# Kernel tuning notes

Measured on AMD Instinct MI355X. Metric: run time of the kernel, lower is better.

Reference implementation:

```python
import jax, jax.numpy as jnp
import numpy as np

N_NODES, N_EDGES, FEA_DIM, H_DIM, N_LAYER, N_GRAPHS, LABEL_DIM = 50000, 600000, 128, 256, 3, 256, 2


def setup_inputs() -> dict:
    key = jax.random.key(0)
    ks = jax.random.split(key, 8)
    x = jax.random.normal(ks[0], (N_NODES, FEA_DIM), jnp.float32)
    edge_index = jax.random.randint(ks[1], (2, N_EDGES), 0, N_NODES, dtype=jnp.int64)
    batch = jnp.sort(jax.random.randint(ks[2], (N_NODES,), 0, N_GRAPHS, dtype=jnp.int64))
    Wg = jax.random.normal(ks[3], (N_LAYER, FEA_DIM, FEA_DIM), jnp.float32) / np.sqrt(FEA_DIM)
    bg = jnp.zeros((N_LAYER, FEA_DIM), jnp.float32)
    w1 = jax.random.normal(ks[4], (FEA_DIM, H_DIM), jnp.float32) / np.sqrt(FEA_DIM)
    b1 = jnp.zeros((H_DIM,), jnp.float32)
    w2 = jax.random.normal(ks[5], (H_DIM, LABEL_DIM), jnp.float32) / np.sqrt(H_DIM)
    b2 = jnp.zeros((LABEL_DIM,), jnp.float32)
    return dict(x=x, Wg=Wg, bg=bg, w1=w1, b1=b1, w2=w2, b2=b2,
                edge_index=edge_index, batch=batch)


def reference(x, Wg, bg, w1, b1, w2, b2, edge_index, batch):
    N = x.shape[0]
    # --- GCN normalization with self-loops (PyG GCNConv default) ---
    loop = jnp.arange(N, dtype=edge_index.dtype)
    src = jnp.concatenate([edge_index[0], loop])  # [E+N]
    dst = jnp.concatenate([edge_index[1], loop])
    deg = jax.ops.segment_sum(jnp.ones_like(src, x.dtype), dst, num_segments=N)
    dinv = jnp.where(deg > 0, jax.lax.rsqrt(jnp.maximum(deg, 1.0)), 0.0)
    norm = dinv[src] * dinv[dst]  # [E+N]
    # --- stacked GCNConv + ReLU ---
    for l in range(Wg.shape[0]):
        h = x @ Wg[l]                              # [N, D] linear transform
        msg = h[src] * norm[:, None]               # gather + edge scale
        x = jax.ops.segment_sum(msg, dst, num_segments=N) + bg[l]  # scatter-add
        x = jax.nn.relu(x)
    # --- global mean pool over graphs ---
    sums = jax.ops.segment_sum(x, batch, num_segments=N_GRAPHS)
    counts = jax.ops.segment_sum(jnp.ones((N, 1), x.dtype), batch, num_segments=N_GRAPHS)
    pooled = sums / jnp.maximum(counts, 1.0)       # [G, D]
    # --- MLP head ---
    h = jax.nn.relu(pooled @ w1 + b1)
    return h @ w2 + b2                             # [G, label_dim]
```

## Files before the change

kernel.cpp:

```cpp
#include <hip/hip_runtime.h>
#include <hip/hip_bf16.h>

#define N_NODES 50000
#define N_EDGES 600000
#define FEA_DIM 128
#define H_DIM 256
#define N_LAYER 3
#define N_GRAPHS 256
#define LABEL_DIM 2

#define SCAN_NB ((N_NODES + 255) / 256)
#define GEMM_NB ((N_NODES + 63) / 64)
#define EDGE_NB ((N_EDGES + 255) / 256)
#define AGG_NB (((N_NODES + 7) / 8) * 2)


__global__ __launch_bounds__(256) void k_count(const int* __restrict__ dst, int* __restrict__ counts) {
    int e = blockIdx.x * 256 + threadIdx.x;
    if (e < N_EDGES) atomicAdd(&counts[dst[e]], 1);
}


__device__ __forceinline__ void gemm_body(const float* __restrict__ X, const float* __restrict__ W,
                                          float* __restrict__ H, int M, int tile) {
    __shared__ float a_s[32][68];
    __shared__ float b_s[32][128];
    const int tid = threadIdx.x;
    const int row_g = tid >> 4;
    const int col_g = tid & 15;
    const int row_base = tile * 64;
    float acc[4][8] = {};

    for (int kt = 0; kt < 4; ++kt) {
        const int k0 = kt * 32;
#pragma unroll
        for (int j = 0; j < 2; ++j) {
            int id = tid + j * 256;
            int m = id >> 3;
            int kq = (id & 7) << 2;
            float4 v = make_float4(0.f, 0.f, 0.f, 0.f);
            int gr = row_base + m;
            if (gr < M) v = *(const float4*)(X + gr * 128 + k0 + kq);
            a_s[kq + 0][m] = v.x; a_s[kq + 1][m] = v.y;
            a_s[kq + 2][m] = v.z; a_s[kq + 3][m] = v.w;
        }
#pragma unroll
        for (int j = 0; j < 4; ++j) {
            int id = tid + j * 256;
            int k = id >> 5;
            int n = (id & 31) << 2;
            *(float4*)(&b_s[k][n]) = *(const float4*)(W + (k0 + k) * 128 + n);
        }
        __syncthreads();
#pragma unroll 8
        for (int k = 0; k < 32; ++k) {
            float4 a0 = *(const float4*)(&a_s[k][row_g * 4]);
            float4 b0 = *(const float4*)(&b_s[k][col_g * 4]);
            float4 b1 = *(const float4*)(&b_s[k][64 + col_g * 4]);
            float av[4] = {a0.x, a0.y, a0.z, a0.w};
            float bv[8] = {b0.x, b0.y, b0.z, b0.w, b1.x, b1.y, b1.z, b1.w};
#pragma unroll
            for (int i = 0; i < 4; ++i)
#pragma unroll
                for (int jj = 0; jj < 8; ++jj) acc[i][jj] += av[i] * bv[jj];
        }
        __syncthreads();
    }
#pragma unroll
    for (int i = 0; i < 4; ++i) {
        int gr = row_base + row_g * 4 + i;
        if (gr < M) {
            float4 o0 = {acc[i][0], acc[i][1], acc[i][2], acc[i][3]};
            float4 o1 = {acc[i][4], acc[i][5], acc[i][6], acc[i][7]};
            *(float4*)(H + gr * 128 + col_g * 4) = o0;
            *(float4*)(H + gr * 128 + 64 + col_g * 4) = o1;
        }
    }
}

__global__ __launch_bounds__(256) void k_gemm(const float* __restrict__ X, const float* __restrict__ W,
                                              float* __restrict__ H, int M) {
    gemm_body(X, W, H, M, blockIdx.x);
}

__global__ __launch_bounds__(256) void k_gemm0_fill(const float* __restrict__ X, const float* __restrict__ W,
                                                    float* __restrict__ H,
                                                    const int* __restrict__ src, const int* __restrict__ dst,
                                                    const int* __restrict__ row_ptr, int* __restrict__ cursor,
                                                    int* __restrict__ col) {
    if (blockIdx.x < GEMM_NB) {
        gemm_body(X, W, H, N_NODES, blockIdx.x);
    } else {
        int e = (blockIdx.x - GEMM_NB) * 256 + threadIdx.x;
        if (e < N_EDGES) {
            int s = src[e], d = dst[e];
            int p = row_ptr[d] + atomicAdd(&cursor[d], 1);
            col[p] = s;
        }
    }
}


__global__ __launch_bounds__(256) void k_partial(const int* __restrict__ counts, int* __restrict__ partial) {
    int g = blockIdx.x * 256 + threadIdx.x;
    int v = (g < N_NODES) ? counts[g] : 0;
#pragma unroll
    for (int off = 32; off > 0; off >>= 1) v += __shfl_down(v, off);
    __shared__ int ws[4];
    int lane = threadIdx.x & 63, wid = threadIdx.x >> 6;
    if (lane == 0) ws[wid] = v;
    __syncthreads();
    if (threadIdx.x == 0) partial[blockIdx.x] = ws[0] + ws[1] + ws[2] + ws[3];
}

__global__ __launch_bounds__(256) void k_rowptr(const int* __restrict__ counts, const int* __restrict__ partial,
                                                int* __restrict__ row_ptr, float* __restrict__ dinv,
                                                int* __restrict__ cursor) {
    __shared__ int sp[256];
    __shared__ int s[256];
    int tid = threadIdx.x;
    sp[tid] = (tid < SCAN_NB) ? partial[tid] : 0;
    __syncthreads();
#pragma unroll
    for (int off = 1; off < 256; off <<= 1) {
        int t = (tid >= off) ? sp[tid - off] : 0;
        __syncthreads();
        sp[tid] += t;
        __syncthreads();
    }
    int block_off = (blockIdx.x == 0) ? 0 : sp[blockIdx.x - 1];

    int g = blockIdx.x * 256 + tid;
    int c = (g < N_NODES) ? counts[g] : 0;
    s[tid] = c;
    __syncthreads();
#pragma unroll
    for (int off = 1; off < 256; off <<= 1) {
        int t = (tid >= off) ? s[tid - off] : 0;
        __syncthreads();
        s[tid] += t;
        __syncthreads();
    }
    if (g < N_NODES) {
        row_ptr[g] = block_off + s[tid] - c;
        dinv[g] = rsqrtf((float)c + 1.0f);
        cursor[g] = 0;
    }
    if (blockIdx.x == 0 && tid == 0) row_ptr[N_NODES] = sp[SCAN_NB - 1];
}


__global__ __launch_bounds__(256) void k_agg(const float* __restrict__ H, const float* __restrict__ bgl,
                                             const int* __restrict__ row_ptr, const int* __restrict__ col,
                                             const float* __restrict__ dinv,
                                             float* __restrict__ Xo) {
    const int b = blockIdx.x;
    const int half = b & 1;
    const int unit = threadIdx.x >> 5;
    const int fl = threadIdx.x & 31;
    const int i = (b >> 1) * 8 + unit;
    if (i >= N_NODES) return;
    const int fo = half * 32 + fl;
    const float2* H2 = (const float2*)H;
    const float di = dinv[i];
    float2 h = H2[(size_t)i * 64 + fo];
    float2 acc;
    acc.x = h.x * di * di;
    acc.y = h.y * di * di;
    const int p0 = row_ptr[i], p1 = row_ptr[i + 1];
    for (int base = p0; base < p1; base += 32) {
        int m = p1 - base; if (m > 32) m = 32;
        int sc = 0; float wc = 0.f;
        if (fl < m) { sc = col[base + fl]; wc = dinv[sc] * di; }
        for (int j = 0; j < m; j += 8) {
            int cnt = m - j; if (cnt > 8) cnt = 8;
            float2 hbuf[8]; float wbuf[8];
#pragma unroll
            for (int t = 0; t < 8; ++t) {
                if (t < cnt) {
                    int s = __shfl(sc, j + t, 32);
                    wbuf[t] = __shfl(wc, j + t, 32);
                    hbuf[t] = H2[(size_t)s * 64 + fo];
                }
            }
#pragma unroll
            for (int t = 0; t < 8; ++t) {
                if (t < cnt) {
                    acc.x += hbuf[t].x * wbuf[t];
                    acc.y += hbuf[t].y * wbuf[t];
                }
            }
        }
    }
    float2 bb = ((const float2*)bgl)[fo];
    float2 o;
    o.x = fmaxf(acc.x + bb.x, 0.f);
    o.y = fmaxf(acc.y + bb.y, 0.f);
    ((float2*)Xo)[(size_t)i * 64 + fo] = o;
}


__global__ __launch_bounds__(256) void k_poolmlp(const float* __restrict__ X, const int* __restrict__ batch,
                                                 const float* __restrict__ w1, const float* __restrict__ b1,
                                                 const float* __restrict__ w2, const float* __restrict__ b2,
                                                 float* __restrict__ out) {
    __shared__ int s_lo, s_hi;
    __shared__ float red[256];
    __shared__ float xs[128];
    __shared__ float hs[256];
    int g = blockIdx.x, tid = threadIdx.x;
    if (tid == 0) {
        int lo = 0, hi = N_NODES;
        while (lo < hi) { int mid = (lo + hi) >> 1; if (batch[mid] < g) lo = mid + 1; else hi = mid; }
        s_lo = lo;
        int lo2 = lo, hi2 = N_NODES;
        while (lo2 < hi2) { int mid = (lo2 + hi2) >> 1; if (batch[mid] < g + 1) lo2 = mid + 1; else hi2 = mid; }
        s_hi = lo2;
    }
    __syncthreads();
    int lo = s_lo, hi = s_hi;
    int f = tid & 127, half = tid >> 7;
    float acc = 0.f;
    for (int r = lo + half; r < hi; r += 2) acc += X[r * 128 + f];
    red[tid] = acc;
    __syncthreads();
    if (tid < 128) {
        int cnt = hi - lo;
        xs[tid] = (red[tid] + red[tid + 128]) / (float)(cnt > 0 ? cnt : 1);
    }
    __syncthreads();
    float a1 = b1[tid];
#pragma unroll 8
    for (int k = 0; k < 128; ++k) a1 += xs[k] * w1[k * H_DIM + tid];
    hs[tid] = fmaxf(a1, 0.f);
    __syncthreads();
    int j = tid >> 7, t2 = tid & 127;
    float p = hs[t2] * w2[t2 * LABEL_DIM + j] + hs[t2 + 128] * w2[(t2 + 128) * LABEL_DIM + j];
    red[tid] = p;
    __syncthreads();
    for (int s2 = 64; s2 > 0; s2 >>= 1) {
        if (t2 < s2) red[tid] += red[tid + s2];
        __syncthreads();
    }
    if (t2 == 0) out[g * LABEL_DIM + j] = red[tid] + b2[j];
}


extern "C" void kernel_launch(void* const* d_in, const int* in_sizes, int n_in,
                              void* d_out, int out_size, void* d_ws, size_t ws_size,
                              hipStream_t stream) {
    const float* x   = (const float*)d_in[0];
    const float* Wg  = (const float*)d_in[1];
    const float* bg  = (const float*)d_in[2];
    const float* w1  = (const float*)d_in[3];
    const float* b1  = (const float*)d_in[4];
    const float* w2  = (const float*)d_in[5];
    const float* b2  = (const float*)d_in[6];
    const int* eidx  = (const int*)d_in[7];
    const int* batch = (const int*)d_in[8];
    float* out = (float*)d_out;

    const int* src = eidx;
    const int* dst = eidx + N_EDGES;

    char* ws = (char*)d_ws;
    size_t off = 0;
    float* A = (float*)(ws + off); off += (size_t)N_NODES * FEA_DIM * 4;
    float* B = (float*)(ws + off); off += (size_t)N_NODES * FEA_DIM * 4;
    int*   col = (int*)(ws + off); off += (size_t)N_EDGES * 4;
    int*   row_ptr = (int*)(ws + off); off += 200704;
    int*   cursor  = (int*)(ws + off); off += 200704;
    int*   counts  = (int*)(ws + off); off += 200704;
    float* dinv    = (float*)(ws + off); off += 200704;
    int*   partial = (int*)(ws + off); off += 4096;

    hipMemsetAsync(counts, 0, 200704, stream);
    k_count<<<EDGE_NB, 256, 0, stream>>>(dst, counts);
    k_partial<<<SCAN_NB, 256, 0, stream>>>(counts, partial);
    k_rowptr<<<SCAN_NB, 256, 0, stream>>>(counts, partial, row_ptr, dinv, cursor);
    k_gemm0_fill<<<GEMM_NB + EDGE_NB, 256, 0, stream>>>(x, Wg, B, src, dst, row_ptr, cursor, col);

    k_agg<<<AGG_NB, 256, 0, stream>>>(B, bg + 0 * FEA_DIM, row_ptr, col, dinv, A);
    for (int l = 1; l < N_LAYER; ++l) {
        k_gemm<<<GEMM_NB, 256, 0, stream>>>(A, Wg + (size_t)l * FEA_DIM * FEA_DIM, B, N_NODES);
        k_agg<<<AGG_NB, 256, 0, stream>>>(B, bg + (size_t)l * FEA_DIM, row_ptr, col, dinv, A);
    }
    k_poolmlp<<<N_GRAPHS, 256, 0, stream>>>(A, batch, w1, b1, w2, b2, out);
}
```

Measured before the change: 374.9 us.

## Store GEMM output in feature-chunked planes and split aggregation across eight chunks

The GEMM now writes H as eight planes of 16 floats per node, each plane covering all nodes, instead of row-major 128-wide rows. The aggregation kernel assigns each block one 16-float feature chunk for 32 nodes, so each node is handled by an 8-lane group. Each gathered neighbour row is a contiguous 64-byte segment within a plane. This aims to keep a plane's working set (about 3.2 MB) resident in cache during the random gathers. In exchange, each gather fetches less data per transaction, the edge-list and dinv reads are repeated eight times per node, and the loop walks neighbours in chunks of 8.

```diff
diff --git a/kernel.cpp b/kernel.cpp
--- a/kernel.cpp
+++ b/kernel.cpp
@@ -12,7 +12,7 @@
 #define SCAN_NB ((N_NODES + 255) / 256)
 #define GEMM_NB ((N_NODES + 63) / 64)
 #define EDGE_NB ((N_EDGES + 255) / 256)
-#define AGG_NB (((N_NODES + 7) / 8) * 2)
+#define AGG_NB (((N_NODES + 31) / 32) * 8)
 
 
 __global__ __launch_bounds__(256) void k_count(const int* __restrict__ dst, int* __restrict__ counts) {
@@ -66,14 +66,16 @@
         }
         __syncthreads();
     }
+    const int p0 = col_g >> 2;
+    const int o0 = (col_g & 3) * 4;
 #pragma unroll
     for (int i = 0; i < 4; ++i) {
         int gr = row_base + row_g * 4 + i;
         if (gr < M) {
-            float4 o0 = {acc[i][0], acc[i][1], acc[i][2], acc[i][3]};
-            float4 o1 = {acc[i][4], acc[i][5], acc[i][6], acc[i][7]};
-            *(float4*)(H + gr * 128 + col_g * 4) = o0;
-            *(float4*)(H + gr * 128 + 64 + col_g * 4) = o1;
+            float4 v0 = {acc[i][0], acc[i][1], acc[i][2], acc[i][3]};
+            float4 v1 = {acc[i][4], acc[i][5], acc[i][6], acc[i][7]};
+            *(float4*)(H + ((size_t)p0 * N_NODES + gr) * 16 + o0) = v0;
+            *(float4*)(H + ((size_t)(p0 + 4) * N_NODES + gr) * 16 + o0) = v1;
         }
     }
 }
@@ -155,43 +157,40 @@
                                              const float* __restrict__ dinv,
                                              float* __restrict__ Xo) {
     const int b = blockIdx.x;
-    const int half = b & 1;
-    const int unit = threadIdx.x >> 5;
-    const int fl = threadIdx.x & 31;
-    const int i = (b >> 1) * 8 + unit;
+    const int e8 = b & 7;
+    const int unit = threadIdx.x >> 3;
+    const int fl = threadIdx.x & 7;
+    const int i = (b >> 3) * 32 + unit;
     if (i >= N_NODES) return;
-    const int fo = half * 32 + fl;
-    const float2* H2 = (const float2*)H;
+    const float2* Hp = (const float2*)(H + (size_t)e8 * N_NODES * 16);
     const float di = dinv[i];
-    float2 h = H2[(size_t)i * 64 + fo];
+    float2 h = Hp[i * 8 + fl];
     float2 acc;
     acc.x = h.x * di * di;
     acc.y = h.y * di * di;
     const int p0 = row_ptr[i], p1 = row_ptr[i + 1];
-    for (int base = p0; base < p1; base += 32) {
-        int m = p1 - base; if (m > 32) m = 32;
+    for (int base = p0; base < p1; base += 8) {
+        int m = p1 - base; if (m > 8) m = 8;
         int sc = 0; float wc = 0.f;
         if (fl < m) { sc = col[base + fl]; wc = dinv[sc] * di; }
-        for (int j = 0; j < m; j += 8) {
-            int cnt = m - j; if (cnt > 8) cnt = 8;
-            float2 hbuf[8]; float wbuf[8];
-#pragma unroll
-            for (int t = 0; t < 8; ++t) {
-                if (t < cnt) {
-                    int s = __shfl(sc, j + t, 32);
-                    wbuf[t] = __shfl(wc, j + t, 32);
-                    hbuf[t] = H2[(size_t)s * 64 + fo];
-                }
+        float2 hbuf[8]; float wbuf[8];
+#pragma unroll
+        for (int t = 0; t < 8; ++t) {
+            if (t < m) {
+                int s = __shfl(sc, t, 8);
+                wbuf[t] = __shfl(wc, t, 8);
+                hbuf[t] = Hp[s * 8 + fl];
             }
-#pragma unroll
-            for (int t = 0; t < 8; ++t) {
-                if (t < cnt) {
-                    acc.x += hbuf[t].x * wbuf[t];
-                    acc.y += hbuf[t].y * wbuf[t];
-                }
+        }
+#pragma unroll
+        for (int t = 0; t < 8; ++t) {
+            if (t < m) {
+                acc.x += hbuf[t].x * wbuf[t];
+                acc.y += hbuf[t].y * wbuf[t];
             }
         }
     }
+    const int fo = e8 * 8 + fl;
     float2 bb = ((const float2*)bgl)[fo];
     float2 o;
     o.x = fmaxf(acc.x + bb.x, 0.f);
```

Measured after the change: 412.1 us. 1.1x slower.

## Store GEMM output in feature-panel layout and precompute edge weights

Applied to the files above, without the earlier changes.

The GEMM now writes H as four 32-float column panels, each holding all nodes, and the aggregation kernel assigns one panel per block with 16 lanes per node. Each gather of a neighbor row then touches a 128-byte contiguous slice inside a smaller panel, which is meant to improve cache locality for the random gathers. Per-edge normalization weights are also computed once during CSR fill and stored, so the aggregation no longer does a dependent dinv[src] lookup. The cost is an extra 600K-float weight array and more blocks for aggregation. The output of aggregation stays row-major because the next GEMM reads it that way.

```diff
diff --git a/kernel.cpp b/kernel.cpp
--- a/kernel.cpp
+++ b/kernel.cpp
@@ -12,7 +12,7 @@
 #define SCAN_NB ((N_NODES + 255) / 256)
 #define GEMM_NB ((N_NODES + 63) / 64)
 #define EDGE_NB ((N_EDGES + 255) / 256)
-#define AGG_NB (((N_NODES + 7) / 8) * 2)
+#define AGG_NB ((N_NODES / 16) * 4)
 
 
 __global__ __launch_bounds__(256) void k_count(const int* __restrict__ dst, int* __restrict__ counts) {
@@ -66,14 +66,17 @@
         }
         __syncthreads();
     }
+    const int c0 = col_g * 4;
+    const int p0 = c0 >> 5;
+    const int o0 = c0 & 31;
 #pragma unroll
     for (int i = 0; i < 4; ++i) {
         int gr = row_base + row_g * 4 + i;
         if (gr < M) {
-            float4 o0 = {acc[i][0], acc[i][1], acc[i][2], acc[i][3]};
-            float4 o1 = {acc[i][4], acc[i][5], acc[i][6], acc[i][7]};
-            *(float4*)(H + gr * 128 + col_g * 4) = o0;
-            *(float4*)(H + gr * 128 + 64 + col_g * 4) = o1;
+            float4 v0 = {acc[i][0], acc[i][1], acc[i][2], acc[i][3]};
+            float4 v1 = {acc[i][4], acc[i][5], acc[i][6], acc[i][7]};
+            *(float4*)(H + ((size_t)p0 * N_NODES + gr) * 32 + o0) = v0;
+            *(float4*)(H + ((size_t)(p0 + 2) * N_NODES + gr) * 32 + o0) = v1;
         }
     }
 }
@@ -87,7 +90,8 @@
                                                     float* __restrict__ H,
                                                     const int* __restrict__ src, const int* __restrict__ dst,
                                                     const int* __restrict__ row_ptr, int* __restrict__ cursor,
-                                                    int* __restrict__ col) {
+                                                    int* __restrict__ col, float* __restrict__ wts,
+                                                    const float* __restrict__ dinv) {
     if (blockIdx.x < GEMM_NB) {
         gemm_body(X, W, H, N_NODES, blockIdx.x);
     } else {
@@ -96,6 +100,7 @@
             int s = src[e], d = dst[e];
             int p = row_ptr[d] + atomicAdd(&cursor[d], 1);
             col[p] = s;
+            wts[p] = dinv[s] * dinv[d];
         }
     }
 }
@@ -152,35 +157,33 @@
 
 __global__ __launch_bounds__(256) void k_agg(const float* __restrict__ H, const float* __restrict__ bgl,
                                              const int* __restrict__ row_ptr, const int* __restrict__ col,
-                                             const float* __restrict__ dinv,
+                                             const float* __restrict__ wts, const float* __restrict__ dinv,
                                              float* __restrict__ Xo) {
     const int b = blockIdx.x;
-    const int half = b & 1;
-    const int unit = threadIdx.x >> 5;
-    const int fl = threadIdx.x & 31;
-    const int i = (b >> 1) * 8 + unit;
-    if (i >= N_NODES) return;
-    const int fo = half * 32 + fl;
-    const float2* H2 = (const float2*)H;
+    const int pl = b & 3;
+    const int unit = threadIdx.x >> 4;
+    const int fl = threadIdx.x & 15;
+    const int i = (b >> 2) * 16 + unit;
+    const float2* Hp = (const float2*)(H + (size_t)pl * N_NODES * 32);
     const float di = dinv[i];
-    float2 h = H2[(size_t)i * 64 + fo];
+    float2 h = Hp[(size_t)i * 16 + fl];
     float2 acc;
     acc.x = h.x * di * di;
     acc.y = h.y * di * di;
     const int p0 = row_ptr[i], p1 = row_ptr[i + 1];
-    for (int base = p0; base < p1; base += 32) {
-        int m = p1 - base; if (m > 32) m = 32;
+    for (int base = p0; base < p1; base += 16) {
+        int m = p1 - base; if (m > 16) m = 16;
         int sc = 0; float wc = 0.f;
-        if (fl < m) { sc = col[base + fl]; wc = dinv[sc] * di; }
+        if (fl < m) { sc = col[base + fl]; wc = wts[base + fl]; }
         for (int j = 0; j < m; j += 8) {
             int cnt = m - j; if (cnt > 8) cnt = 8;
             float2 hbuf[8]; float wbuf[8];
 #pragma unroll
             for (int t = 0; t < 8; ++t) {
                 if (t < cnt) {
-                    int s = __shfl(sc, j + t, 32);
-                    wbuf[t] = __shfl(wc, j + t, 32);
-                    hbuf[t] = H2[(size_t)s * 64 + fo];
+                    int s = __shfl(sc, j + t, 16);
+                    wbuf[t] = __shfl(wc, j + t, 16);
+                    hbuf[t] = Hp[(size_t)s * 16 + fl];
                 }
             }
 #pragma unroll
@@ -192,6 +195,7 @@
             }
         }
     }
+    const int fo = pl * 16 + fl;
     float2 bb = ((const float2*)bgl)[fo];
     float2 o;
     o.x = fmaxf(acc.x + bb.x, 0.f);
@@ -268,6 +272,7 @@
     float* A = (float*)(ws + off); off += (size_t)N_NODES * FEA_DIM * 4;
     float* B = (float*)(ws + off); off += (size_t)N_NODES * FEA_DIM * 4;
     int*   col = (int*)(ws + off); off += (size_t)N_EDGES * 4;
+    float* wts = (float*)(ws + off); off += (size_t)N_EDGES * 4;
     int*   row_ptr = (int*)(ws + off); off += 200704;
     int*   cursor  = (int*)(ws + off); off += 200704;
     int*   counts  = (int*)(ws + off); off += 200704;
@@ -278,12 +283,12 @@
     k_count<<<EDGE_NB, 256, 0, stream>>>(dst, counts);
     k_partial<<<SCAN_NB, 256, 0, stream>>>(counts, partial);
     k_rowptr<<<SCAN_NB, 256, 0, stream>>>(counts, partial, row_ptr, dinv, cursor);
-    k_gemm0_fill<<<GEMM_NB + EDGE_NB, 256, 0, stream>>>(x, Wg, B, src, dst, row_ptr, cursor, col);
-
-    k_agg<<<AGG_NB, 256, 0, stream>>>(B, bg + 0 * FEA_DIM, row_ptr, col, dinv, A);
+    k_gemm0_fill<<<GEMM_NB + EDGE_NB, 256, 0, stream>>>(x, Wg, B, src, dst, row_ptr, cursor, col, wts, dinv);
+
+    k_agg<<<AGG_NB, 256, 0, stream>>>(B, bg + 0 * FEA_DIM, row_ptr, col, wts, dinv, A);
     for (int l = 1; l < N_LAYER; ++l) {
         k_gemm<<<GEMM_NB, 256, 0, stream>>>(A, Wg + (size_t)l * FEA_DIM * FEA_DIM, B, N_NODES);
-        k_agg<<<AGG_NB, 256, 0, stream>>>(B, bg + (size_t)l * FEA_DIM, row_ptr, col, dinv, A);
+        k_agg<<<AGG_NB, 256, 0, stream>>>(B, bg + (size_t)l * FEA_DIM, row_ptr, col, wts, dinv, A);
     }
     k_poolmlp<<<N_GRAPHS, 256, 0, stream>>>(A, batch, w1, b1, w2, b2, out);
 }
```

New measurement: 421.0 us. +12.3%, slower.

## Sort nodes by degree for aggregation and cache edge weights across layers

Applied to the files above, without the earlier changes.

Builds a degree-bucketed permutation of nodes (histogram, scan, scatter fused into existing kernels) so aggregation processes nodes of similar degree together, reducing wavefront divergence. The first layer's aggregation also stores per-edge normalization weights, which later layers read instead of gathering dinv randomly. The permutation loses output write locality and adds a small scan kernel launch.

```diff
diff --git a/kernel.cpp b/kernel.cpp
--- a/kernel.cpp
+++ b/kernel.cpp
@@ -13,6 +13,7 @@
 #define GEMM_NB ((N_NODES + 63) / 64)
 #define EDGE_NB ((N_EDGES + 255) / 256)
 #define AGG_NB (((N_NODES + 7) / 8) * 2)
+#define NBUCKET 64
 
 
 __global__ __launch_bounds__(256) void k_count(const int* __restrict__ dst, int* __restrict__ counts) {
@@ -87,23 +88,38 @@
                                                     float* __restrict__ H,
                                                     const int* __restrict__ src, const int* __restrict__ dst,
                                                     const int* __restrict__ row_ptr, int* __restrict__ cursor,
-                                                    int* __restrict__ col) {
+                                                    int* __restrict__ col,
+                                                    const int* __restrict__ counts,
+                                                    const int* __restrict__ pbase, int* __restrict__ pcur,
+                                                    int* __restrict__ perm) {
     if (blockIdx.x < GEMM_NB) {
         gemm_body(X, W, H, N_NODES, blockIdx.x);
-    } else {
+    } else if (blockIdx.x < GEMM_NB + EDGE_NB) {
         int e = (blockIdx.x - GEMM_NB) * 256 + threadIdx.x;
         if (e < N_EDGES) {
             int s = src[e], d = dst[e];
             int p = row_ptr[d] + atomicAdd(&cursor[d], 1);
             col[p] = s;
         }
-    }
-}
-
-
-__global__ __launch_bounds__(256) void k_partial(const int* __restrict__ counts, int* __restrict__ partial) {
+    } else {
+        int g = (blockIdx.x - GEMM_NB - EDGE_NB) * 256 + threadIdx.x;
+        if (g < N_NODES) {
+            int d = counts[g]; if (d > NBUCKET - 1) d = NBUCKET - 1;
+            int pos = pbase[d] + atomicAdd(&pcur[d], 1);
+            perm[pos] = g;
+        }
+    }
+}
+
+
+__global__ __launch_bounds__(256) void k_partial(const int* __restrict__ counts, int* __restrict__ partial,
+                                                 int* __restrict__ hist) {
     int g = blockIdx.x * 256 + threadIdx.x;
     int v = (g < N_NODES) ? counts[g] : 0;
+    if (g < N_NODES) {
+        int d = v; if (d > NBUCKET - 1) d = NBUCKET - 1;
+        atomicAdd(&hist[d], 1);
+    }
 #pragma unroll
     for (int off = 32; off > 0; off >>= 1) v += __shfl_down(v, off);
     __shared__ int ws[4];
@@ -149,17 +165,36 @@
     if (blockIdx.x == 0 && tid == 0) row_ptr[N_NODES] = sp[SCAN_NB - 1];
 }
 
-
-__global__ __launch_bounds__(256) void k_agg(const float* __restrict__ H, const float* __restrict__ bgl,
-                                             const int* __restrict__ row_ptr, const int* __restrict__ col,
-                                             const float* __restrict__ dinv,
-                                             float* __restrict__ Xo) {
+__global__ __launch_bounds__(64) void k_permscan(const int* __restrict__ hist, int* __restrict__ pbase) {
+    __shared__ int sh[NBUCKET];
+    int tid = threadIdx.x;
+    int h = hist[tid];
+    sh[tid] = h;
+    __syncthreads();
+#pragma unroll
+    for (int off = 1; off < NBUCKET; off <<= 1) {
+        int t = (tid >= off) ? sh[tid - off] : 0;
+        __syncthreads();
+        sh[tid] += t;
+        __syncthreads();
+    }
+    pbase[tid] = sh[tid] - h;
+}
+
+
+template <int L0>
+__global__ __launch_bounds__(256) void k_agg_t(const float* __restrict__ H, const float* __restrict__ bgl,
+                                               const int* __restrict__ row_ptr, const int* __restrict__ col,
+                                               float* __restrict__ wts, const float* __restrict__ dinv,
+                                               const int* __restrict__ perm,
+                                               float* __restrict__ Xo) {
     const int b = blockIdx.x;
     const int half = b & 1;
     const int unit = threadIdx.x >> 5;
     const int fl = threadIdx.x & 31;
-    const int i = (b >> 1) * 8 + unit;
-    if (i >= N_NODES) return;
+    const int idx = (b >> 1) * 8 + unit;
+    if (idx >= N_NODES) return;
+    const int i = perm[idx];
     const int fo = half * 32 + fl;
     const float2* H2 = (const float2*)H;
     const float di = dinv[i];
@@ -171,7 +206,15 @@
     for (int base = p0; base < p1; base += 32) {
         int m = p1 - base; if (m > 32) m = 32;
         int sc = 0; float wc = 0.f;
-        if (fl < m) { sc = col[base + fl]; wc = dinv[sc] * di; }
+        if (fl < m) {
+            sc = col[base + fl];
+            if (L0) {
+                wc = dinv[sc] * di;
+                if (half == 0) wts[base + fl] = wc;
+            } else {
+                wc = wts[base + fl];
+            }
+        }
         for (int j = 0; j < m; j += 8) {
             int cnt = m - j; if (cnt > 8) cnt = 8;
             float2 hbuf[8]; float wbuf[8];
@@ -268,22 +311,29 @@
     float* A = (float*)(ws + off); off += (size_t)N_NODES * FEA_DIM * 4;
     float* B = (float*)(ws + off); off += (size_t)N_NODES * FEA_DIM * 4;
     int*   col = (int*)(ws + off); off += (size_t)N_EDGES * 4;
+    float* wts = (float*)(ws + off); off += (size_t)N_EDGES * 4;
     int*   row_ptr = (int*)(ws + off); off += 200704;
     int*   cursor  = (int*)(ws + off); off += 200704;
     int*   counts  = (int*)(ws + off); off += 200704;
+    int*   hist    = (int*)(ws + off); off += 512;
+    int*   pcur    = (int*)(ws + off); off += 512;
     float* dinv    = (float*)(ws + off); off += 200704;
     int*   partial = (int*)(ws + off); off += 4096;
-
-    hipMemsetAsync(counts, 0, 200704, stream);
+    int*   pbase   = (int*)(ws + off); off += 512;
+    int*   perm    = (int*)(ws + off); off += 200704;
+
+    hipMemsetAsync(counts, 0, 200704 + 1024, stream);
     k_count<<<EDGE_NB, 256, 0, stream>>>(dst, counts);
-    k_partial<<<SCAN_NB, 256, 0, stream>>>(counts, partial);
+    k_partial<<<SCAN_NB, 256, 0, stream>>>(counts, partial, hist);
     k_rowptr<<<SCAN_NB, 256, 0, stream>>>(counts, partial, row_ptr, dinv, cursor);
-    k_gemm0_fill<<<GEMM_NB + EDGE_NB, 256, 0, stream>>>(x, Wg, B, src, dst, row_ptr, cursor, col);
-
-    k_agg<<<AGG_NB, 256, 0, stream>>>(B, bg + 0 * FEA_DIM, row_ptr, col, dinv, A);
+    k_permscan<<<1, 64, 0, stream>>>(hist, pbase);
+    k_gemm0_fill<<<GEMM_NB + EDGE_NB + SCAN_NB, 256, 0, stream>>>(x, Wg, B, src, dst, row_ptr, cursor, col,
+                                                                  counts, pbase, pcur, perm);
+
+    k_agg_t<1><<<AGG_NB, 256, 0, stream>>>(B, bg + 0 * FEA_DIM, row_ptr, col, wts, dinv, perm, A);
     for (int l = 1; l < N_LAYER; ++l) {
         k_gemm<<<GEMM_NB, 256, 0, stream>>>(A, Wg + (size_t)l * FEA_DIM * FEA_DIM, B, N_NODES);
-        k_agg<<<AGG_NB, 256, 0, stream>>>(B, bg + (size_t)l * FEA_DIM, row_ptr, col, dinv, A);
+        k_agg_t<0><<<AGG_NB, 256, 0, stream>>>(B, bg + (size_t)l * FEA_DIM, row_ptr, col, wts, dinv, perm, A);
     }
     k_poolmlp<<<N_GRAPHS, 256, 0, stream>>>(A, batch, w1, b1, w2, b2, out);
 }
```

After: 706.9 us. 88.5% more time.
